# Kernel tuning notes

Measured on AMD Instinct MI355X. Metric: run time of the kernel, lower is better.

## Reference

```python
import jax, jax.numpy as jnp
import numpy as np

BERT_DIM = 768
N_ROWS = 5
N_COLS = 12
LN_EPS = 1e-5


def setup_inputs() -> dict:
    key = jax.random.key(0)
    ks = jax.random.split(key, 12)
    B, S = 256, 512
    token_hidden = jax.random.normal(ks[0], (B, S, BERT_DIM), dtype=jnp.float32)
    attention_mask = jax.random.randint(ks[1], (B, S), 0, 2, dtype=jnp.int32)
    s = lambda fan_in: 1.0 / np.sqrt(fan_in)
    return {
        "token_hidden": token_hidden,
        "attention_mask": attention_mask,
        # token_attention: Linear(768,128) -> Tanh -> Linear(128,1)
        "att_w1": jax.random.normal(ks[2], (128, BERT_DIM), dtype=jnp.float32) * s(BERT_DIM),
        "att_b1": jnp.zeros((128,), dtype=jnp.float32),
        "att_w2": jax.random.normal(ks[3], (1, 128), dtype=jnp.float32) * s(128),
        "att_b2": jnp.zeros((1,), dtype=jnp.float32),
        # feature_projector: Linear(768,256) -> GELU -> Dropout(eval) -> Linear(256,5)
        "proj_w1": jax.random.normal(ks[4], (256, BERT_DIM), dtype=jnp.float32) * s(BERT_DIM),
        "proj_b1": jnp.zeros((256,), dtype=jnp.float32),
        "proj_w2": jax.random.normal(ks[5], (N_ROWS, 256), dtype=jnp.float32) * s(256),
        "proj_b2": jnp.zeros((N_ROWS,), dtype=jnp.float32),
        # LayerNorm([5, 12])
        "ln_gamma": jnp.ones((N_ROWS, N_COLS), dtype=jnp.float32),
        "ln_beta": jnp.zeros((N_ROWS, N_COLS), dtype=jnp.float32),
    }


def reference(token_hidden, attention_mask, att_w1, att_b1, att_w2, att_b2,
              proj_w1, proj_b1, proj_w2, proj_b2, ln_gamma, ln_beta):
    # token attention scores: [B, S]
    h = jnp.tanh(jnp.einsum("bsd,hd->bsh", token_hidden, att_w1) + att_b1)
    scores = (jnp.einsum("bsh,oh->bso", h, att_w2) + att_b2)[..., 0]
    scores = jnp.where(attention_mask == 0, jnp.finfo(scores.dtype).min, scores)
    weights = jax.nn.softmax(scores, axis=-1)
    # top-k token selection (indices sorted ascending to preserve order)
    k = min(N_COLS, token_hidden.shape[1])
    _, top_idx = jax.lax.top_k(weights, k)  # [B, k]
    top_idx = jnp.sort(top_idx, axis=-1)
    selected = jnp.take_along_axis(token_hidden, top_idx[:, :, None], axis=1)  # [B, k, D]
    # feature projector (dropout is eval no-op)
    f = jax.nn.gelu(jnp.einsum("bkd,hd->bkh", selected, proj_w1) + proj_b1, approximate=False)
    f = jnp.einsum("bkh,rh->bkr", f, proj_w2) + proj_b2  # [B, k, n_rows]
    features = jnp.transpose(f, (0, 2, 1))  # [B, n_rows, k]
    if features.shape[-1] < N_COLS:
        features = jnp.pad(features, ((0, 0), (0, 0), (0, N_COLS - features.shape[-1])))
    # LayerNorm over trailing [n_rows, n_cols]
    mean = jnp.mean(features, axis=(-2, -1), keepdims=True)
    var = jnp.var(features, axis=(-2, -1), keepdims=True)
    return ln_gamma * (features - mean) * jax.lax.rsqrt(var + LN_EPS) + ln_beta
```

## Files before the change

kernel.cpp:

```cpp
#include <hip/hip_runtime.h>
#include <math.h>

#define B_BATCH 256
#define S_LEN   512
#define D_DIM   768
#define H_ATT   128
#define TOPK    12
#define H_PROJ  256
#define N_ROWS  5
#define N_COLS  12

#define BM 128
#define BK 16

__global__ __launch_bounds__(256) void score_kernel(
    const float* __restrict__ th,
    const float* __restrict__ w1,
    const float* __restrict__ b1,
    const float* __restrict__ w2,
    float* __restrict__ scores)
{
    __shared__ float As[BK][BM + 4];
    __shared__ float Bs[BK][H_ATT + 4];
    __shared__ float red[BM][17];

    const int tid   = threadIdx.x;
    const int m_blk = blockIdx.x * BM;
    const int tm = tid >> 4;
    const int tn = tid & 15;
    const int m0 = tm * 8;
    const int j0 = tn * 8;

    float acc[8][8];
#pragma unroll
    for (int i = 0; i < 8; ++i)
#pragma unroll
        for (int j = 0; j < 8; ++j) acc[i][j] = 0.0f;

    for (int k0 = 0; k0 < D_DIM; k0 += BK) {
#pragma unroll
        for (int i = 0; i < 2; ++i) {
            int f   = tid * 2 + i;
            int row = f >> 2;
            int c4  = f & 3;
            float4 v = *(const float4*)(th + (size_t)(m_blk + row) * D_DIM + k0 + c4 * 4);
            int kk = c4 * 4;
            As[kk + 0][row] = v.x; As[kk + 1][row] = v.y;
            As[kk + 2][row] = v.z; As[kk + 3][row] = v.w;
        }
#pragma unroll
        for (int i = 0; i < 2; ++i) {
            int f   = tid * 2 + i;
            int row = f >> 2;
            int c4  = f & 3;
            float4 v = *(const float4*)(w1 + (size_t)row * D_DIM + k0 + c4 * 4);
            int kk = c4 * 4;
            Bs[kk + 0][row] = v.x; Bs[kk + 1][row] = v.y;
            Bs[kk + 2][row] = v.z; Bs[kk + 3][row] = v.w;
        }
        __syncthreads();

#pragma unroll
        for (int k = 0; k < BK; ++k) {
            float a[8], b[8];
            *(float4*)&a[0] = *(const float4*)&As[k][m0];
            *(float4*)&a[4] = *(const float4*)&As[k][m0 + 4];
            *(float4*)&b[0] = *(const float4*)&Bs[k][j0];
            *(float4*)&b[4] = *(const float4*)&Bs[k][j0 + 4];
#pragma unroll
            for (int i = 0; i < 8; ++i)
#pragma unroll
                for (int j = 0; j < 8; ++j) acc[i][j] += a[i] * b[j];
        }
        __syncthreads();
    }

    float b1r[8], w2r[8];
#pragma unroll
    for (int j = 0; j < 8; ++j) { b1r[j] = b1[j0 + j]; w2r[j] = w2[j0 + j]; }

#pragma unroll
    for (int i = 0; i < 8; ++i) {
        float s = 0.0f;
#pragma unroll
        for (int j = 0; j < 8; ++j) s += tanhf(acc[i][j] + b1r[j]) * w2r[j];
        red[m0 + i][tn] = s;
    }
    __syncthreads();

    if (tid < BM) {
        float s = 0.0f;
#pragma unroll
        for (int t = 0; t < 16; ++t) s += red[tid][t];
        scores[m_blk + tid] = s;
    }
}

__global__ __launch_bounds__(256) void select_project_kernel(
    const float* __restrict__ th,
    const int*   __restrict__ mask,
    const float* __restrict__ scores,
    const float* __restrict__ pw1,
    const float* __restrict__ pb1,
    const float* __restrict__ pw2,
    const float* __restrict__ pb2,
    const float* __restrict__ gamma,
    const float* __restrict__ beta,
    float* __restrict__ out)
{
    const int b   = blockIdx.x;
    const int tid = threadIdx.x;

    __shared__ float sc[S_LEN];
    __shared__ int   sel[TOPK];
    __shared__ float xsel[TOPK][D_DIM];
    __shared__ float gbuf[TOPK][H_PROJ + 1];
    __shared__ float rv[256];
    __shared__ int   ri[256];
    __shared__ float feat[N_ROWS * N_COLS];
    __shared__ float stats[2];

    const float NEG_MIN = -3.402823466e38f;

    for (int i = tid; i < S_LEN; i += 256) {
        float s = scores[(size_t)b * S_LEN + i];
        sc[i] = (mask[(size_t)b * S_LEN + i] == 0) ? NEG_MIN : s;
    }
    __syncthreads();

    for (int it = 0; it < TOPK; ++it) {
        float best = -INFINITY; int bi = 1 << 30;
        for (int i = tid; i < S_LEN; i += 256) {
            float v = sc[i];
            if (v > best || (v == best && i < bi)) { best = v; bi = i; }
        }
        rv[tid] = best; ri[tid] = bi;
        __syncthreads();
        for (int s = 128; s > 0; s >>= 1) {
            if (tid < s) {
                float ov = rv[tid + s]; int oi = ri[tid + s];
                if (ov > rv[tid] || (ov == rv[tid] && oi < ri[tid])) {
                    rv[tid] = ov; ri[tid] = oi;
                }
            }
            __syncthreads();
        }
        if (tid == 0) { sel[it] = ri[0]; sc[ri[0]] = -INFINITY; }
        __syncthreads();
    }

    if (tid == 0) {
        for (int i = 1; i < TOPK; ++i) {
            int k = sel[i], j = i - 1;
            while (j >= 0 && sel[j] > k) { sel[j + 1] = sel[j]; --j; }
            sel[j + 1] = k;
        }
    }
    __syncthreads();

    for (int f = tid; f < TOPK * (D_DIM / 4); f += 256) {
        int t = f / (D_DIM / 4);
        int c = f % (D_DIM / 4);
        ((float4*)xsel[t])[c] =
            ((const float4*)(th + ((size_t)b * S_LEN + sel[t]) * D_DIM))[c];
    }
    __syncthreads();

    {
        const int j = tid;
        float acc[TOPK];
        float bj = pb1[j];
#pragma unroll
        for (int t = 0; t < TOPK; ++t) acc[t] = bj;
        const float4* wrow = (const float4*)(pw1 + (size_t)j * D_DIM);
        for (int k4 = 0; k4 < D_DIM / 4; ++k4) {
            float4 w = wrow[k4];
#pragma unroll
            for (int t = 0; t < TOPK; ++t) {
                float4 x = ((const float4*)xsel[t])[k4];
                acc[t] += w.x * x.x + w.y * x.y + w.z * x.z + w.w * x.w;
            }
        }
#pragma unroll
        for (int t = 0; t < TOPK; ++t) {
            float h = acc[t];
            float g = 0.5f * h * (1.0f + erff(h * 0.70710678118654752f));
            gbuf[t][j] = g;
        }
    }
    __syncthreads();

    if (tid < TOPK * N_ROWS) {
        int t = tid / N_ROWS, r = tid % N_ROWS;
        float s = pb2[r];
        for (int j = 0; j < H_PROJ; ++j) s += gbuf[t][j] * pw2[r * H_PROJ + j];
        feat[r * N_COLS + t] = s;
    }
    __syncthreads();

    if (tid == 0) {
        float sum = 0.0f;
        for (int i = 0; i < N_ROWS * N_COLS; ++i) sum += feat[i];
        float mean = sum / (float)(N_ROWS * N_COLS);
        float sq = 0.0f;
        for (int i = 0; i < N_ROWS * N_COLS; ++i) {
            float d = feat[i] - mean; sq += d * d;
        }
        stats[0] = mean;
        stats[1] = sq / (float)(N_ROWS * N_COLS);
    }
    __syncthreads();

    if (tid < N_ROWS * N_COLS) {
        float x = feat[tid];
        float y = gamma[tid] * (x - stats[0]) * rsqrtf(stats[1] + 1e-5f) + beta[tid];
        out[(size_t)b * (N_ROWS * N_COLS) + tid] = y;
    }
}

extern "C" void kernel_launch(void* const* d_in, const int* in_sizes, int n_in,
                              void* d_out, int out_size, void* d_ws, size_t ws_size,
                              hipStream_t stream) {
    const float* th    = (const float*)d_in[0];
    const int*   mask  = (const int*)  d_in[1];
    const float* aw1   = (const float*)d_in[2];
    const float* ab1   = (const float*)d_in[3];
    const float* aw2   = (const float*)d_in[4];
    const float* pw1   = (const float*)d_in[6];
    const float* pb1   = (const float*)d_in[7];
    const float* pw2   = (const float*)d_in[8];
    const float* pb2   = (const float*)d_in[9];
    const float* gam   = (const float*)d_in[10];
    const float* bet   = (const float*)d_in[11];
    float* out = (float*)d_out;

    float* scores = (float*)d_ws;

    const int M = B_BATCH * S_LEN;
    hipLaunchKernelGGL(score_kernel, dim3(M / BM), dim3(256), 0, stream,
                       th, aw1, ab1, aw2, scores);
    hipLaunchKernelGGL(select_project_kernel, dim3(B_BATCH), dim3(256), 0, stream,
                       th, mask, scores, pw1, pb1, pw2, pb2, gam, bet, out);
}
```

Measured before the change: 801.3 us.

## Compute attention scores with split-bf16 MFMA and rescore top candidates exactly

Replaces the fp32 SIMT score GEMM with an MFMA kernel that splits inputs and weights into hi/lo bf16 pairs and runs three MFMAs per tile to approximate fp32. A prep kernel repacks the attention weights into MFMA-friendly layouts each call. Because the approximate scores could reorder close tokens, the select kernel takes 16 candidates, recomputes their scores exactly in fp32, then picks the top 12. The top-k search also switches to packed 64-bit keys reduced with wave shuffles. The cost is extra kernels and a possible mismatch if a true top-12 token falls outside the 16 candidates.

```diff
diff --git a/kernel.cpp b/kernel.cpp
--- a/kernel.cpp
+++ b/kernel.cpp
@@ -6,100 +6,165 @@
 #define D_DIM   768
 #define H_ATT   128
 #define TOPK    12
+#define NCAND   16
 #define H_PROJ  256
 #define N_ROWS  5
 #define N_COLS  12
 
-#define BM 128
-#define BK 16
-
-__global__ __launch_bounds__(256) void score_kernel(
-    const float* __restrict__ th,
-    const float* __restrict__ w1,
-    const float* __restrict__ b1,
-    const float* __restrict__ w2,
+typedef __bf16 bf16x4 __attribute__((ext_vector_type(4)));
+typedef __bf16 bf16x8 __attribute__((ext_vector_type(8)));
+typedef float  f32x4  __attribute__((ext_vector_type(4)));
+
+#define WS_SCORES 0
+#define WS_WHI    524288
+#define WS_WLO    720896
+#define WS_W1Q    917504
+
+__global__ __launch_bounds__(256) void prep_kernel(
+    const float* __restrict__ w1, __bf16* __restrict__ whi,
+    __bf16* __restrict__ wlo, float* __restrict__ w1q)
+{
+    int id = blockIdx.x * 256 + threadIdx.x;
+    if (id < 98304) {
+        int j    = id & 7;
+        int lane = (id >> 3) & 63;
+        int rest = id >> 9;
+        int kt   = rest % 24;
+        int nt   = rest / 24;
+        int n = nt * 16 + (lane & 15);
+        int k = kt * 32 + (lane >> 4) * 8 + j;
+        float f = w1[n * D_DIM + k];
+        __bf16 h = (__bf16)f;
+        whi[id] = h;
+        wlo[id] = (__bf16)(f - (float)h);
+    } else {
+        int e2 = id - 98304;
+        int i  = e2 & 3;
+        int n  = (e2 >> 2) & 127;
+        int k4 = e2 >> 9;
+        w1q[e2] = w1[n * D_DIM + k4 * 4 + i];
+    }
+}
+
+__global__ __launch_bounds__(256, 3) void score_mfma(
+    const float*  __restrict__ th,
+    const __bf16* __restrict__ whi,
+    const __bf16* __restrict__ wlo,
+    const float*  __restrict__ b1,
+    const float*  __restrict__ w2,
     float* __restrict__ scores)
 {
-    __shared__ float As[BK][BM + 4];
-    __shared__ float Bs[BK][H_ATT + 4];
-    __shared__ float red[BM][17];
-
-    const int tid   = threadIdx.x;
-    const int m_blk = blockIdx.x * BM;
-    const int tm = tid >> 4;
-    const int tn = tid & 15;
-    const int m0 = tm * 8;
-    const int j0 = tn * 8;
-
-    float acc[8][8];
-#pragma unroll
-    for (int i = 0; i < 8; ++i)
-#pragma unroll
-        for (int j = 0; j < 8; ++j) acc[i][j] = 0.0f;
-
-    for (int k0 = 0; k0 < D_DIM; k0 += BK) {
-#pragma unroll
-        for (int i = 0; i < 2; ++i) {
-            int f   = tid * 2 + i;
-            int row = f >> 2;
-            int c4  = f & 3;
-            float4 v = *(const float4*)(th + (size_t)(m_blk + row) * D_DIM + k0 + c4 * 4);
-            int kk = c4 * 4;
-            As[kk + 0][row] = v.x; As[kk + 1][row] = v.y;
-            As[kk + 2][row] = v.z; As[kk + 3][row] = v.w;
-        }
-#pragma unroll
-        for (int i = 0; i < 2; ++i) {
-            int f   = tid * 2 + i;
-            int row = f >> 2;
-            int c4  = f & 3;
-            float4 v = *(const float4*)(w1 + (size_t)row * D_DIM + k0 + c4 * 4);
-            int kk = c4 * 4;
-            Bs[kk + 0][row] = v.x; Bs[kk + 1][row] = v.y;
-            Bs[kk + 2][row] = v.z; Bs[kk + 3][row] = v.w;
+    __shared__ __bf16 Ah[8 * 512];
+    __shared__ __bf16 Al[8 * 512];
+    __shared__ __bf16 Bh[8 * 512];
+    __shared__ __bf16 Bl[8 * 512];
+
+    const int tid = threadIdx.x;
+    const int wv  = tid >> 6;
+    const int ln  = tid & 63;
+    const int mblk = blockIdx.x * 128;
+
+    f32x4 acc[2][8];
+    const f32x4 z = {0.f, 0.f, 0.f, 0.f};
+#pragma unroll
+    for (int i = 0; i < 2; ++i)
+#pragma unroll
+        for (int j = 0; j < 8; ++j) acc[i][j] = z;
+
+    for (int kt = 0; kt < 24; ++kt) {
+        float4 v[4];
+#pragma unroll
+        for (int i = 0; i < 4; ++i) {
+            int f = tid + 256 * i;
+            int row = f >> 3, q = f & 7;
+            v[i] = *(const float4*)(th + (size_t)(mblk + row) * D_DIM + kt * 32 + q * 4);
+        }
+        uint4 bb[4];
+#pragma unroll
+        for (int i = 0; i < 4; ++i) {
+            int f = tid + 256 * i;
+            int r = f & 511;
+            int nt = r >> 6, l = r & 63;
+            const __bf16* src = (f >> 9) ? wlo : whi;
+            bb[i] = *(const uint4*)(src + ((size_t)(nt * 24 + kt) * 64 + l) * 8);
         }
         __syncthreads();
 
 #pragma unroll
-        for (int k = 0; k < BK; ++k) {
-            float a[8], b[8];
-            *(float4*)&a[0] = *(const float4*)&As[k][m0];
-            *(float4*)&a[4] = *(const float4*)&As[k][m0 + 4];
-            *(float4*)&b[0] = *(const float4*)&Bs[k][j0];
-            *(float4*)&b[4] = *(const float4*)&Bs[k][j0 + 4];
-#pragma unroll
-            for (int i = 0; i < 8; ++i)
-#pragma unroll
-                for (int j = 0; j < 8; ++j) acc[i][j] += a[i] * b[j];
+        for (int i = 0; i < 4; ++i) {
+            int f = tid + 256 * i;
+            int row = f >> 3, q = f & 7;
+            int mt = row >> 4, kq = q >> 1;
+            int l16 = (row & 15) | (kq << 4);
+            int a16 = l16 ^ (kq << 2);
+            __bf16 h0 = (__bf16)v[i].x, h1 = (__bf16)v[i].y;
+            __bf16 h2 = (__bf16)v[i].z, h3 = (__bf16)v[i].w;
+            bf16x4 hv = {h0, h1, h2, h3};
+            bf16x4 lv = {(__bf16)(v[i].x - (float)h0), (__bf16)(v[i].y - (float)h1),
+                         (__bf16)(v[i].z - (float)h2), (__bf16)(v[i].w - (float)h3)};
+            int off = mt * 512 + a16 * 8 + (q & 1) * 4;
+            *(bf16x4*)(&Ah[off]) = hv;
+            *(bf16x4*)(&Al[off]) = lv;
+        }
+#pragma unroll
+        for (int i = 0; i < 4; ++i) {
+            int f = tid + 256 * i;
+            int r = f & 511;
+            int nt = r >> 6, l = r & 63;
+            __bf16* dst = (f >> 9) ? Bl : Bh;
+            *(uint4*)(&dst[nt * 512 + l * 8]) = bb[i];
         }
         __syncthreads();
-    }
-
-    float b1r[8], w2r[8];
-#pragma unroll
-    for (int j = 0; j < 8; ++j) { b1r[j] = b1[j0 + j]; w2r[j] = w2[j0 + j]; }
-
-#pragma unroll
-    for (int i = 0; i < 8; ++i) {
-        float s = 0.0f;
-#pragma unroll
-        for (int j = 0; j < 8; ++j) s += tanhf(acc[i][j] + b1r[j]) * w2r[j];
-        red[m0 + i][tn] = s;
-    }
-    __syncthreads();
-
-    if (tid < BM) {
-        float s = 0.0f;
-#pragma unroll
-        for (int t = 0; t < 16; ++t) s += red[tid][t];
-        scores[m_blk + tid] = s;
-    }
+
+        const int al = ln ^ (((ln >> 4) & 3) << 2);
+        bf16x8 ah0 = *(bf16x8*)(&Ah[(wv * 2 + 0) * 512 + al * 8]);
+        bf16x8 ah1 = *(bf16x8*)(&Ah[(wv * 2 + 1) * 512 + al * 8]);
+        bf16x8 al0 = *(bf16x8*)(&Al[(wv * 2 + 0) * 512 + al * 8]);
+        bf16x8 al1 = *(bf16x8*)(&Al[(wv * 2 + 1) * 512 + al * 8]);
+#pragma unroll
+        for (int nt = 0; nt < 8; ++nt) {
+            bf16x8 bh = *(bf16x8*)(&Bh[nt * 512 + ln * 8]);
+            bf16x8 bl = *(bf16x8*)(&Bl[nt * 512 + ln * 8]);
+            acc[0][nt] = __builtin_amdgcn_mfma_f32_16x16x32_bf16(ah0, bh, acc[0][nt], 0, 0, 0);
+            acc[0][nt] = __builtin_amdgcn_mfma_f32_16x16x32_bf16(ah0, bl, acc[0][nt], 0, 0, 0);
+            acc[0][nt] = __builtin_amdgcn_mfma_f32_16x16x32_bf16(al0, bh, acc[0][nt], 0, 0, 0);
+            acc[1][nt] = __builtin_amdgcn_mfma_f32_16x16x32_bf16(ah1, bh, acc[1][nt], 0, 0, 0);
+            acc[1][nt] = __builtin_amdgcn_mfma_f32_16x16x32_bf16(ah1, bl, acc[1][nt], 0, 0, 0);
+            acc[1][nt] = __builtin_amdgcn_mfma_f32_16x16x32_bf16(al1, bh, acc[1][nt], 0, 0, 0);
+        }
+    }
+
+    const int col = ln & 15;
+    float b1v[8], w2v[8];
+#pragma unroll
+    for (int nt = 0; nt < 8; ++nt) {
+        b1v[nt] = b1[nt * 16 + col];
+        w2v[nt] = w2[nt * 16 + col];
+    }
+#pragma unroll
+    for (int mf = 0; mf < 2; ++mf)
+#pragma unroll
+        for (int r = 0; r < 4; ++r) {
+            float s = 0.f;
+#pragma unroll
+            for (int nt = 0; nt < 8; ++nt)
+                s += tanhf(acc[mf][nt][r] + b1v[nt]) * w2v[nt];
+            s += __shfl_xor(s, 1, 64);
+            s += __shfl_xor(s, 2, 64);
+            s += __shfl_xor(s, 4, 64);
+            s += __shfl_xor(s, 8, 64);
+            if (col == 0)
+                scores[mblk + wv * 32 + mf * 16 + (ln >> 4) * 4 + r] = s;
+        }
 }
 
-__global__ __launch_bounds__(256) void select_project_kernel(
+__global__ __launch_bounds__(256) void select_kernel(
     const float* __restrict__ th,
     const int*   __restrict__ mask,
-    const float* __restrict__ scores,
+    const float* __restrict__ ascores,
+    const float* __restrict__ w1q,
+    const float* __restrict__ ab1,
+    const float* __restrict__ aw2,
     const float* __restrict__ pw1,
     const float* __restrict__ pb1,
     const float* __restrict__ pw2,
@@ -110,82 +175,143 @@
 {
     const int b   = blockIdx.x;
     const int tid = threadIdx.x;
-
+    const int wv  = tid >> 6;
+    const int ln  = tid & 63;
+
+    __shared__ float4 xc[NCAND][192];
     __shared__ float sc[S_LEN];
-    __shared__ int   sel[TOPK];
-    __shared__ float xsel[TOPK][D_DIM];
+    __shared__ unsigned long long wbest[4];
+    __shared__ int   cand[NCAND];
+    __shared__ float redW[4][8];
+    __shared__ float exact_sc[NCAND];
+    __shared__ int   sel_slot[TOPK];
     __shared__ float gbuf[TOPK][H_PROJ + 1];
-    __shared__ float rv[256];
-    __shared__ int   ri[256];
     __shared__ float feat[N_ROWS * N_COLS];
     __shared__ float stats[2];
 
     const float NEG_MIN = -3.402823466e38f;
 
     for (int i = tid; i < S_LEN; i += 256) {
-        float s = scores[(size_t)b * S_LEN + i];
+        float s = ascores[(size_t)b * S_LEN + i];
         sc[i] = (mask[(size_t)b * S_LEN + i] == 0) ? NEG_MIN : s;
     }
     __syncthreads();
 
-    for (int it = 0; it < TOPK; ++it) {
-        float best = -INFINITY; int bi = 1 << 30;
-        for (int i = tid; i < S_LEN; i += 256) {
-            float v = sc[i];
-            if (v > best || (v == best && i < bi)) { best = v; bi = i; }
-        }
-        rv[tid] = best; ri[tid] = bi;
+    for (int it = 0; it < NCAND; ++it) {
+        float v0 = sc[tid], v1 = sc[tid + 256];
+        unsigned k0 = __float_as_uint(v0);
+        k0 = ((int)k0 >= 0) ? (k0 | 0x80000000u) : ~k0;
+        unsigned k1 = __float_as_uint(v1);
+        k1 = ((int)k1 >= 0) ? (k1 | 0x80000000u) : ~k1;
+        unsigned long long p0 = ((unsigned long long)k0 << 32) | (0xFFFFFFFFu - (unsigned)tid);
+        unsigned long long p1 = ((unsigned long long)k1 << 32) | (0xFFFFFFFFu - (unsigned)(tid + 256));
+        unsigned long long best = p0 > p1 ? p0 : p1;
+#pragma unroll
+        for (int m = 1; m <= 32; m <<= 1) {
+            unsigned long long o = __shfl_xor(best, m, 64);
+            if (o > best) best = o;
+        }
+        if (ln == 0) wbest[wv] = best;
         __syncthreads();
-        for (int s = 128; s > 0; s >>= 1) {
-            if (tid < s) {
-                float ov = rv[tid + s]; int oi = ri[tid + s];
-                if (ov > rv[tid] || (ov == rv[tid] && oi < ri[tid])) {
-                    rv[tid] = ov; ri[tid] = oi;
-                }
+        if (tid == 0) {
+            unsigned long long bb = wbest[0];
+            for (int w = 1; w < 4; ++w) if (wbest[w] > bb) bb = wbest[w];
+            int idx = (int)(0xFFFFFFFFu - (unsigned)(bb & 0xFFFFFFFFu));
+            cand[it] = idx;
+            sc[idx] = -INFINITY;
+        }
+        __syncthreads();
+    }
+
+#pragma unroll
+    for (int i = 0; i < 12; ++i) {
+        int f = tid + 256 * i;
+        int c = f / 192, k4 = f % 192;
+        xc[c][k4] = *(const float4*)(th + ((size_t)b * S_LEN + cand[c]) * D_DIM + k4 * 4);
+    }
+    __syncthreads();
+
+    {
+        const int n = tid & 127;
+        const int h = tid >> 7;
+        float accs[8];
+#pragma unroll
+        for (int ci = 0; ci < 8; ++ci) accs[ci] = 0.f;
+        for (int k4 = 0; k4 < 192; ++k4) {
+            float4 w = *(const float4*)(w1q + (size_t)(k4 * 128 + n) * 4);
+#pragma unroll
+            for (int ci = 0; ci < 8; ++ci) {
+                float4 x = xc[2 * ci + h][k4];
+                accs[ci] += w.x * x.x + w.y * x.y + w.z * x.z + w.w * x.w;
             }
-            __syncthreads();
-        }
-        if (tid == 0) { sel[it] = ri[0]; sc[ri[0]] = -INFINITY; }
-        __syncthreads();
-    }
+        }
+        float b1n = ab1[n], w2n = aw2[n];
+#pragma unroll
+        for (int ci = 0; ci < 8; ++ci) {
+            float val = tanhf(accs[ci] + b1n) * w2n;
+            val += __shfl_xor(val, 1, 64);
+            val += __shfl_xor(val, 2, 64);
+            val += __shfl_xor(val, 4, 64);
+            val += __shfl_xor(val, 8, 64);
+            val += __shfl_xor(val, 16, 64);
+            val += __shfl_xor(val, 32, 64);
+            if (ln == 0) redW[wv][ci] = val;
+        }
+    }
+    __syncthreads();
+    if (tid < NCAND) {
+        int c = tid;
+        float ex = (c & 1) ? (redW[2][c >> 1] + redW[3][c >> 1])
+                           : (redW[0][c >> 1] + redW[1][c >> 1]);
+        if (mask[(size_t)b * S_LEN + cand[c]] == 0) ex = -INFINITY;
+        exact_sc[c] = ex;
+    }
+    __syncthreads();
 
     if (tid == 0) {
+        unsigned picked = 0;
+        int slots[TOPK];
+        for (int it = 0; it < TOPK; ++it) {
+            float best = -INFINITY; int bslot = -1; int bidx = 1 << 30;
+            for (int c = 0; c < NCAND; ++c) {
+                if (picked & (1u << c)) continue;
+                float e = exact_sc[c]; int idx = cand[c];
+                if (e > best || (e == best && idx < bidx)) { best = e; bslot = c; bidx = idx; }
+            }
+            picked |= 1u << bslot;
+            slots[it] = bslot;
+        }
         for (int i = 1; i < TOPK; ++i) {
-            int k = sel[i], j = i - 1;
-            while (j >= 0 && sel[j] > k) { sel[j + 1] = sel[j]; --j; }
-            sel[j + 1] = k;
-        }
-    }
-    __syncthreads();
-
-    for (int f = tid; f < TOPK * (D_DIM / 4); f += 256) {
-        int t = f / (D_DIM / 4);
-        int c = f % (D_DIM / 4);
-        ((float4*)xsel[t])[c] =
-            ((const float4*)(th + ((size_t)b * S_LEN + sel[t]) * D_DIM))[c];
+            int s = slots[i], key = cand[s], j = i - 1;
+            while (j >= 0 && cand[slots[j]] > key) { slots[j + 1] = slots[j]; --j; }
+            slots[j + 1] = s;
+        }
+        for (int t = 0; t < TOPK; ++t) sel_slot[t] = slots[t];
     }
     __syncthreads();
 
     {
         const int j = tid;
-        float acc[TOPK];
+        int slots[TOPK];
+#pragma unroll
+        for (int t = 0; t < TOPK; ++t) slots[t] = sel_slot[t];
+        float accp[TOPK];
         float bj = pb1[j];
 #pragma unroll
-        for (int t = 0; t < TOPK; ++t) acc[t] = bj;
+        for (int t = 0; t < TOPK; ++t) accp[t] = bj;
         const float4* wrow = (const float4*)(pw1 + (size_t)j * D_DIM);
-        for (int k4 = 0; k4 < D_DIM / 4; ++k4) {
+        for (int k4 = 0; k4 < 192; ++k4) {
             float4 w = wrow[k4];
 #pragma unroll
             for (int t = 0; t < TOPK; ++t) {
-                float4 x = ((const float4*)xsel[t])[k4];
-                acc[t] += w.x * x.x + w.y * x.y + w.z * x.z + w.w * x.w;
+                float4 x = xc[slots[t]][k4];
+                accp[t] += w.x * x.x + w.y * x.y + w.z * x.z + w.w * x.w;
             }
         }
 #pragma unroll
         for (int t = 0; t < TOPK; ++t) {
-            float h = acc[t];
-            float g = 0.5f * h * (1.0f + erff(h * 0.70710678118654752f));
-            gbuf[t][j] = g;
+            float hh = accp[t];
+            gbuf[t][j] = 0.5f * hh * (1.0f + erff(hh * 0.70710678118654752f));
         }
     }
     __syncthreads();
@@ -199,46 +325,49 @@
     __syncthreads();
 
     if (tid == 0) {
-        float sum = 0.0f;
+        float sum = 0.f;
         for (int i = 0; i < N_ROWS * N_COLS; ++i) sum += feat[i];
-        float mean = sum / (float)(N_ROWS * N_COLS);
-        float sq = 0.0f;
-        for (int i = 0; i < N_ROWS * N_COLS; ++i) {
-            float d = feat[i] - mean; sq += d * d;
-        }
+        float mean = sum / 60.f;
+        float sq = 0.f;
+        for (int i = 0; i < N_ROWS * N_COLS; ++i) { float d = feat[i] - mean; sq += d * d; }
         stats[0] = mean;
-        stats[1] = sq / (float)(N_ROWS * N_COLS);
-    }
-    __syncthreads();
-
+        stats[1] = sq / 60.f;
+    }
+    __syncthreads();
     if (tid < N_ROWS * N_COLS) {
         float x = feat[tid];
-        float y = gamma[tid] * (x - stats[0]) * rsqrtf(stats[1] + 1e-5f) + beta[tid];
-        out[(size_t)b * (N_ROWS * N_COLS) + tid] = y;
+        out[(size_t)b * 60 + tid] =
+            gamma[tid] * (x - stats[0]) * rsqrtf(stats[1] + 1e-5f) + beta[tid];
     }
 }
 
 extern "C" void kernel_launch(void* const* d_in, const int* in_sizes, int n_in,
                               void* d_out, int out_size, void* d_ws, size_t ws_size,
                               hipStream_t stream) {
-    const float* th    = (const float*)d_in[0];
-    const int*   mask  = (const int*)  d_in[1];
-    const float* aw1   = (const float*)d_in[2];
-    const float* ab1   = (const float*)d_in[3];
-    const float* aw2   = (const float*)d_in[4];
-    const float* pw1   = (const float*)d_in[6];
-    const float* pb1   = (const float*)d_in[7];
-    const float* pw2   = (const float*)d_in[8];
-    const float* pb2   = (const float*)d_in[9];
-    const float* gam   = (const float*)d_in[10];
-    const float* bet   = (const float*)d_in[11];
+    const float* th   = (const float*)d_in[0];
+    const int*   mask = (const int*)  d_in[1];
+    const float* aw1  = (const float*)d_in[2];
+    const float* ab1  = (const float*)d_in[3];
+    const float* aw2  = (const float*)d_in[4];
+    const float* pw1  = (const float*)d_in[6];
+    const float* pb1  = (const float*)d_in[7];
+    const float* pw2  = (const float*)d_in[8];
+    const float* pb2  = (const float*)d_in[9];
+    const float* gam  = (const float*)d_in[10];
+    const float* bet  = (const float*)d_in[11];
     float* out = (float*)d_out;
 
-    float* scores = (float*)d_ws;
-
-    const int M = B_BATCH * S_LEN;
-    hipLaunchKernelGGL(score_kernel, dim3(M / BM), dim3(256), 0, stream,
-                       th, aw1, ab1, aw2, scores);
-    hipLaunchKernelGGL(select_project_kernel, dim3(B_BATCH), dim3(256), 0, stream,
-                       th, mask, scores, pw1, pb1, pw2, pb2, gam, bet, out);
+    char* ws = (char*)d_ws;
+    float*  scores = (float*)(ws + WS_SCORES);
+    __bf16* whi    = (__bf16*)(ws + WS_WHI);
+    __bf16* wlo    = (__bf16*)(ws + WS_WLO);
+    float*  w1q    = (float*)(ws + WS_W1Q);
+
+    hipLaunchKernelGGL(prep_kernel, dim3(768), dim3(256), 0, stream,
+                       aw1, whi, wlo, w1q);
+    hipLaunchKernelGGL(score_mfma, dim3(131072 / 128), dim3(256), 0, stream,
+                       th, whi, wlo, ab1, aw2, scores);
+    hipLaunchKernelGGL(select_kernel, dim3(B_BATCH), dim3(256), 0, stream,
+                       th, mask, scores, w1q, ab1, aw2,
+                       pw1, pb1, pw2, pb2, gam, bet, out);
 }
```

Result: faster. 767.7 us (-4.2%).
